# Kernel tuning notes

Measured on AMD Instinct MI355X. Metric: run time of the kernel, lower is better.

## Reference

```python
import jax, jax.numpy as jnp
import numpy as np

INTRINSIC_DIM = 3  # all linear dims, no periodic dims
EPS = 1e-10


def _cdist(a, b):
    # Euclidean distance via the expanded form; clamp for numerical safety.
    sq = (jnp.sum(a * a, axis=1)[:, None]
          + jnp.sum(b * b, axis=1)[None, :]
          - 2.0 * (a @ b.T))
    return jnp.sqrt(jnp.maximum(sq, 0.0))


def _thin_plate_kernel(r, dim):
    r_safe = jnp.maximum(r, EPS)
    if dim == 2:
        k = r_safe ** 2 * jnp.log(r_safe)
    else:
        k = r_safe ** (dim - 2) * jnp.log(r_safe)
    return jnp.where(r < EPS, jnp.zeros_like(k), k)


def setup_inputs() -> dict:
    key = jax.random.key(0)
    k1, k2, k3, k4 = jax.random.split(key, 4)
    batch, n, d, amb = 16384, 4096, INTRINSIC_DIM, 3
    m = 1 + d  # constant + one linear term per (non-periodic) dim
    u = jax.random.uniform(k1, (batch, d), dtype=jnp.float32)
    control_points = jax.random.uniform(k2, (n, d), dtype=jnp.float32)
    rbf_weights = jax.random.normal(k3, (n, amb), dtype=jnp.float32)
    poly_coeffs = jax.random.normal(k4, (m, amb), dtype=jnp.float32)
    return {"u": u, "control_points": control_points,
            "rbf_weights": rbf_weights, "poly_coeffs": poly_coeffs}


def reference(u, control_points, rbf_weights, poly_coeffs):
    # K_query: (batch, n) TPS kernel on pairwise Euclidean distances
    dists = _cdist(u, control_points)
    K_query = _thin_plate_kernel(dists, dim=INTRINSIC_DIM)
    # Polynomial matrix: [1, x] over all linear dims -> (batch, 1 + d)
    P_query = jnp.concatenate([jnp.ones((u.shape[0], 1), dtype=u.dtype), u], axis=1)
    return K_query @ rbf_weights + P_query @ poly_coeffs
```

## Files before the change

### kernel.cpp

```cpp
#include <hip/hip_runtime.h>


#define BLK 1024
#define QPB 64
#define NSPLIT 16

__global__ void pack_kernel(const float* __restrict__ cp,
                            const float* __restrict__ w,
                            float4* __restrict__ pack, int n) {
    const int j = blockIdx.x * blockDim.x + threadIdx.x;
    if (j >= n) return;
    const float C = 0.34657359027997264f;
    const float cx = cp[j * 3 + 0], cy = cp[j * 3 + 1], cz = cp[j * 3 + 2];
    pack[j * 2 + 0] = make_float4(-2.f * cx, -2.f * cy, -2.f * cz,
                                  cx * cx + cy * cy + cz * cz);
    pack[j * 2 + 1] = make_float4(C * w[j * 3 + 0], C * w[j * 3 + 1],
                                  C * w[j * 3 + 2], 0.f);
}

__global__ __launch_bounds__(BLK) void tps_kernel(
    const float* __restrict__ u,
    const float* __restrict__ pack,
    const float* __restrict__ poly,
    float* __restrict__ out,
    int batch, int n)
{
    __shared__ float s_red[NSPLIT][QPB * 3];

    const int tid  = threadIdx.x;
    const int lane = tid & 63;
    const int wid  = __builtin_amdgcn_readfirstlane(tid >> 6);

    const int q  = blockIdx.x * QPB + lane;
    const int ql = q < batch ? q : batch - 1;
    const float ux = u[ql * 3 + 0];
    const float uy = u[ql * 3 + 1];
    const float uz = u[ql * 3 + 2];
    const float usq = fmaf(ux, ux, fmaf(uy, uy, uz * uz));

    float ax = 0.f, ay = 0.f, az = 0.f;
    if (wid == 0) {
        ax = poly[0] + ux * poly[3] + uy * poly[6] + uz * poly[9];
        ay = poly[1] + ux * poly[4] + uy * poly[7] + uz * poly[10];
        az = poly[2] + ux * poly[5] + uy * poly[8] + uz * poly[11];
    }

    const int J0  = (n + NSPLIT - 1) / NSPLIT;
    const int jlo = wid * J0;
    const int jcnt = min(jlo + J0, n) - jlo;
    const float* __restrict__ pj = pack + (size_t)jlo * 8;

#pragma unroll 4
    for (int j = 0; j < jcnt; ++j) {
        const float m2x = pj[j * 8 + 0];
        const float m2y = pj[j * 8 + 1];
        const float m2z = pj[j * 8 + 2];
        const float c2  = pj[j * 8 + 3];
        const float wx  = pj[j * 8 + 4];
        const float wy  = pj[j * 8 + 5];
        const float wz  = pj[j * 8 + 6];

        float r2 = fmaf(m2x, ux, fmaf(m2y, uy, fmaf(m2z, uz, c2 + usq)));
        r2 = fmaxf(r2, 1e-30f);
        const float kk = __builtin_amdgcn_sqrtf(r2) * __builtin_amdgcn_logf(r2);
        ax = fmaf(kk, wx, ax);
        ay = fmaf(kk, wy, ay);
        az = fmaf(kk, wz, az);
    }

    s_red[wid][lane * 3 + 0] = ax;
    s_red[wid][lane * 3 + 1] = ay;
    s_red[wid][lane * 3 + 2] = az;
    __syncthreads();

    if (tid < QPB * 3) {
        float s = 0.f;
#pragma unroll
        for (int w2 = 0; w2 < NSPLIT; ++w2) s += s_red[w2][tid];
        const int qq = blockIdx.x * QPB + tid / 3;
        if (qq < batch) out[(size_t)blockIdx.x * (QPB * 3) + tid] = s;
    }
}

extern "C" void kernel_launch(void* const* d_in, const int* in_sizes, int n_in,
                              void* d_out, int out_size, void* d_ws, size_t ws_size,
                              hipStream_t stream) {
    const float* u    = (const float*)d_in[0];
    const float* cp   = (const float*)d_in[1];
    const float* w    = (const float*)d_in[2];
    const float* poly = (const float*)d_in[3];
    float* out  = (float*)d_out;
    float* pack = (float*)d_ws;

    const int batch = in_sizes[0] / 3;
    const int n     = in_sizes[1] / 3;

    pack_kernel<<<(n + 255) / 256, 256, 0, stream>>>(cp, w, (float4*)pack, n);

    dim3 block(BLK);
    dim3 grid((batch + QPB - 1) / QPB);
    tps_kernel<<<grid, block, 0, stream>>>(u, pack, poly, out, batch, n);
}
```

Baseline: 89.14 us.

## Compute distances and weighted sum with bf16 MFMA using split hi/lo operands

Replaces the scalar per-pair distance loop with two MFMA stages. The first computes squared distances from bf16 hi/lo split coordinates, and the second multiplies the bf16 kernel values by the bf16 weights, staged through LDS. The goal is to move the dot-product and accumulation FLOPs onto matrix cores, leaving only sqrt/log on the vector ALU. This costs precision: kernel values are truncated to bf16, and the code assumes batch divisible by 16 and n by 8*32, with a hardcoded weight stride.

```diff
diff --git a/kernel.cpp b/kernel.cpp
--- a/kernel.cpp
+++ b/kernel.cpp
@@ -1,84 +1,138 @@
 #include <hip/hip_runtime.h>
 
 
-#define BLK 1024
-#define QPB 64
-#define NSPLIT 16
+typedef __attribute__((ext_vector_type(8))) short short8;
+typedef __attribute__((ext_vector_type(4))) float float4v;
+
+#define WT_STRIDE 4104
+
+__device__ inline unsigned short bf16rn(float x) {
+    unsigned u = __float_as_uint(x);
+    return (unsigned short)((u + 0x7FFFu + ((u >> 16) & 1u)) >> 16);
+}
+__device__ inline float bf16tof(unsigned short h) {
+    return __uint_as_float(((unsigned)h) << 16);
+}
 
 __global__ void pack_kernel(const float* __restrict__ cp,
                             const float* __restrict__ w,
-                            float4* __restrict__ pack, int n) {
+                            unsigned short* __restrict__ pack,
+                            unsigned short* __restrict__ wt, int n) {
     const int j = blockIdx.x * blockDim.x + threadIdx.x;
     if (j >= n) return;
     const float C = 0.34657359027997264f;
     const float cx = cp[j * 3 + 0], cy = cp[j * 3 + 1], cz = cp[j * 3 + 2];
-    pack[j * 2 + 0] = make_float4(-2.f * cx, -2.f * cy, -2.f * cz,
-                                  cx * cx + cy * cy + cz * cz);
-    pack[j * 2 + 1] = make_float4(C * w[j * 3 + 0], C * w[j * 3 + 1],
-                                  C * w[j * 3 + 2], 0.f);
+    const unsigned short bh0 = bf16rn(cx), bh1 = bf16rn(cy), bh2 = bf16rn(cz);
+    const unsigned short bl0 = bf16rn(cx - bf16tof(bh0));
+    const unsigned short bl1 = bf16rn(cy - bf16tof(bh1));
+    const unsigned short bl2 = bf16rn(cz - bf16tof(bh2));
+    const float csq = fmaf(cx, cx, fmaf(cy, cy, cz * cz));
+    const unsigned short ch = bf16rn(csq), cl = bf16rn(csq - bf16tof(ch));
+    const unsigned short one = 0x3F80;
+    unsigned short s[16] = {bh0, bh1, bh2, bl0, bl1, bl2, bh0, bh1,
+                            bh2, one, one, ch, cl, 0, 0, 0};
+#pragma unroll
+    for (int t = 0; t < 16; ++t) pack[j * 16 + t] = s[t];
+    wt[0 * WT_STRIDE + j] = bf16rn(C * w[j * 3 + 0]);
+    wt[1 * WT_STRIDE + j] = bf16rn(C * w[j * 3 + 1]);
+    wt[2 * WT_STRIDE + j] = bf16rn(C * w[j * 3 + 2]);
+    wt[3 * WT_STRIDE + j] = 0;
 }
 
-__global__ __launch_bounds__(BLK) void tps_kernel(
+#define BLK 512
+#define NSPLIT 8
+
+__global__ __launch_bounds__(BLK) void tps_mfma(
     const float* __restrict__ u,
-    const float* __restrict__ pack,
+    const unsigned short* __restrict__ pack,
+    const unsigned short* __restrict__ wt,
     const float* __restrict__ poly,
     float* __restrict__ out,
     int batch, int n)
 {
-    __shared__ float s_red[NSPLIT][QPB * 3];
+    __shared__ unsigned short kk[NSPLIT][16 * 40];
+    __shared__ float red[NSPLIT][64][4];
 
     const int tid  = threadIdx.x;
     const int lane = tid & 63;
-    const int wid  = __builtin_amdgcn_readfirstlane(tid >> 6);
+    const int wv   = tid >> 6;
+    const int col  = lane & 15;
+    const int quad = lane >> 4;
 
-    const int q  = blockIdx.x * QPB + lane;
-    const int ql = q < batch ? q : batch - 1;
-    const float ux = u[ql * 3 + 0];
-    const float uy = u[ql * 3 + 1];
-    const float uz = u[ql * 3 + 2];
-    const float usq = fmaf(ux, ux, fmaf(uy, uy, uz * uz));
+    const int qt = blockIdx.x;
 
-    float ax = 0.f, ay = 0.f, az = 0.f;
-    if (wid == 0) {
-        ax = poly[0] + ux * poly[3] + uy * poly[6] + uz * poly[9];
-        ay = poly[1] + ux * poly[4] + uy * poly[7] + uz * poly[10];
-        az = poly[2] + ux * poly[5] + uy * poly[8] + uz * poly[11];
+    const int q_a = qt * 16 + col;
+    const float ax_ = u[q_a * 3 + 0], ay_ = u[q_a * 3 + 1], az_ = u[q_a * 3 + 2];
+    const float m2x = -2.f * ax_, m2y = -2.f * ay_, m2z = -2.f * az_;
+    const unsigned short h0 = bf16rn(m2x), h1 = bf16rn(m2y), h2 = bf16rn(m2z);
+    const unsigned short l0 = bf16rn(m2x - bf16tof(h0));
+    const unsigned short l1 = bf16rn(m2y - bf16tof(h1));
+    const unsigned short l2 = bf16rn(m2z - bf16tof(h2));
+    const float usq = fmaf(ax_, ax_, fmaf(ay_, ay_, az_ * az_));
+    const unsigned short sh = bf16rn(usq), sl = bf16rn(usq - bf16tof(sh));
+    const unsigned short one = 0x3F80;
+
+    short8 a1 = {0, 0, 0, 0, 0, 0, 0, 0};
+    if (quad == 0) {
+        a1[0] = (short)h0; a1[1] = (short)h1; a1[2] = (short)h2;
+        a1[3] = (short)h0; a1[4] = (short)h1; a1[5] = (short)h2;
+        a1[6] = (short)l0; a1[7] = (short)l1;
+    } else if (quad == 1) {
+        a1[0] = (short)l2; a1[1] = (short)sh; a1[2] = (short)sl;
+        a1[3] = (short)one; a1[4] = (short)one;
     }
 
-    const int J0  = (n + NSPLIT - 1) / NSPLIT;
-    const int jlo = wid * J0;
-    const int jcnt = min(jlo + J0, n) - jlo;
-    const float* __restrict__ pj = pack + (size_t)jlo * 8;
+    const float4v zero4 = {0.f, 0.f, 0.f, 0.f};
+    float4v acc = {0.f, 0.f, 0.f, 0.f};
 
-#pragma unroll 4
-    for (int j = 0; j < jcnt; ++j) {
-        const float m2x = pj[j * 8 + 0];
-        const float m2y = pj[j * 8 + 1];
-        const float m2z = pj[j * 8 + 2];
-        const float c2  = pj[j * 8 + 3];
-        const float wx  = pj[j * 8 + 4];
-        const float wy  = pj[j * 8 + 5];
-        const float wz  = pj[j * 8 + 6];
+    const int cstart = wv * (n / NSPLIT);
+    const int cend   = cstart + (n / NSPLIT);
+    unsigned short* kkw = &kk[wv][(quad * 4) * 40 + col];
 
-        float r2 = fmaf(m2x, ux, fmaf(m2y, uy, fmaf(m2z, uz, c2 + usq)));
-        r2 = fmaxf(r2, 1e-30f);
-        const float kk = __builtin_amdgcn_sqrtf(r2) * __builtin_amdgcn_logf(r2);
-        ax = fmaf(kk, wx, ax);
-        ay = fmaf(kk, wy, ay);
-        az = fmaf(kk, wz, az);
+    for (int cb = cstart; cb < cend; cb += 32) {
+        short8 b0 = {0, 0, 0, 0, 0, 0, 0, 0};
+        short8 b1 = {0, 0, 0, 0, 0, 0, 0, 0};
+        if (quad < 2) {
+            b0 = *(const short8*)(pack + (cb + col) * 16 + quad * 8);
+            b1 = *(const short8*)(pack + (cb + 16 + col) * 16 + quad * 8);
+        }
+        float4v r2a = __builtin_amdgcn_mfma_f32_16x16x32_bf16(a1, b0, zero4, 0, 0, 0);
+        float4v r2b = __builtin_amdgcn_mfma_f32_16x16x32_bf16(a1, b1, zero4, 0, 0, 0);
+
+#pragma unroll
+        for (int i = 0; i < 4; ++i) {
+            const float va = fmaxf(r2a[i], 1e-30f);
+            const float vb = fmaxf(r2b[i], 1e-30f);
+            const float ka = __builtin_amdgcn_sqrtf(va) * __builtin_amdgcn_logf(va);
+            const float kb = __builtin_amdgcn_sqrtf(vb) * __builtin_amdgcn_logf(vb);
+            kkw[i * 40 + 0]  = (unsigned short)(__float_as_uint(ka) >> 16);
+            kkw[i * 40 + 16] = (unsigned short)(__float_as_uint(kb) >> 16);
+        }
+
+        short8 a2 = *(const short8*)(&kk[wv][col * 40 + quad * 8]);
+        const int nr = col < 3 ? col : 3;
+        short8 wf = *(const short8*)(wt + nr * WT_STRIDE + cb + quad * 8);
+        acc = __builtin_amdgcn_mfma_f32_16x16x32_bf16(a2, wf, acc, 0, 0, 0);
     }
 
-    s_red[wid][lane * 3 + 0] = ax;
-    s_red[wid][lane * 3 + 1] = ay;
-    s_red[wid][lane * 3 + 2] = az;
+    red[wv][lane][0] = acc[0];
+    red[wv][lane][1] = acc[1];
+    red[wv][lane][2] = acc[2];
+    red[wv][lane][3] = acc[3];
     __syncthreads();
 
-    if (tid < QPB * 3) {
-        float s = 0.f;
+    if (wv == 0 && col < 3) {
 #pragma unroll
-        for (int w2 = 0; w2 < NSPLIT; ++w2) s += s_red[w2][tid];
-        const int qq = blockIdx.x * QPB + tid / 3;
-        if (qq < batch) out[(size_t)blockIdx.x * (QPB * 3) + tid] = s;
+        for (int i = 0; i < 4; ++i) {
+            float s = 0.f;
+#pragma unroll
+            for (int w2 = 0; w2 < NSPLIT; ++w2) s += red[w2][lane][i];
+            const int q = qt * 16 + quad * 4 + i;
+            const float px = u[q * 3 + 0], py = u[q * 3 + 1], pz = u[q * 3 + 2];
+            s += poly[col] + px * poly[3 + col] + py * poly[6 + col]
+                           + pz * poly[9 + col];
+            out[q * 3 + col] = s;
+        }
     }
 }
 
@@ -89,15 +143,17 @@
     const float* cp   = (const float*)d_in[1];
     const float* w    = (const float*)d_in[2];
     const float* poly = (const float*)d_in[3];
-    float* out  = (float*)d_out;
-    float* pack = (float*)d_ws;
+    float* out = (float*)d_out;
 
     const int batch = in_sizes[0] / 3;
     const int n     = in_sizes[1] / 3;
 
-    pack_kernel<<<(n + 255) / 256, 256, 0, stream>>>(cp, w, (float4*)pack, n);
+    unsigned short* pack = (unsigned short*)d_ws;
+    unsigned short* wt   = pack + (size_t)n * 16;
+
+    pack_kernel<<<(n + 255) / 256, 256, 0, stream>>>(cp, w, pack, wt, n);
 
     dim3 block(BLK);
-    dim3 grid((batch + QPB - 1) / QPB);
-    tps_kernel<<<grid, block, 0, stream>>>(u, pack, poly, out, batch, n);
+    dim3 grid(batch / 16);
+    tps_mfma<<<grid, block, 0, stream>>>(u, pack, wt, poly, out, batch, n);
 }
```

Result: faster. 80.49 us (-9.7%).
